# Kernel optimization log

Hardware: AMD Instinct MI355X
Metric: run time of the kernel (lower is better)

The kernel has to match this reference:

```python
import jax, jax.numpy as jnp
import numpy as np

NUM_HEADS = 16
ROPE_BASE = 10000.0


def _rope_cos_sin(T, head_dim, dtype):
    # standard rotary: angles[t, i] = t * base^(-2i/head_dim), half-split layout
    inv_freq = 1.0 / (ROPE_BASE ** (jnp.arange(0, head_dim, 2, dtype=jnp.float32) / head_dim))
    ang = jnp.arange(T, dtype=jnp.float32)[:, None] * inv_freq[None, :]  # [T, hd/2]
    cos = jnp.concatenate([jnp.cos(ang), jnp.cos(ang)], axis=-1).astype(dtype)  # [T, hd]
    sin = jnp.concatenate([jnp.sin(ang), jnp.sin(ang)], axis=-1).astype(dtype)
    return cos, sin


def _rotate_half(t):
    t1, t2 = jnp.split(t, 2, axis=-1)
    return jnp.concatenate([-t2, t1], axis=-1)


def _apply_rope(t, cos, sin):
    # t: [B, H, T, hd]; cos/sin: [T, hd]
    return t * cos[None, None] + _rotate_half(t) * sin[None, None]


def setup_inputs() -> dict:
    key = jax.random.key(0)
    B, T, C = 2, 2048, 1024
    k1, k2, k3 = jax.random.split(key, 3)
    x = jax.random.normal(k1, (B, T, C), dtype=jnp.float32)
    w_attn = jax.random.normal(k2, (C, 3 * C), dtype=jnp.float32) * (C ** -0.5)
    w_proj = jax.random.normal(k3, (C, C), dtype=jnp.float32) * (C ** -0.5)
    return {"x": x, "w_attn": w_attn, "w_proj": w_proj}


def reference(x, w_attn, w_proj):
    B, T, C = x.shape
    H = NUM_HEADS
    hd = C // H

    qkv = x @ w_attn  # [B, T, 3C]
    q, k, v = jnp.split(qkv, 3, axis=-1)
    # [B, T, C] -> [B, H, T, hd]
    q = q.reshape(B, T, H, hd).transpose(0, 2, 1, 3)
    k = k.reshape(B, T, H, hd).transpose(0, 2, 1, 3)
    v = v.reshape(B, T, H, hd).transpose(0, 2, 1, 3)

    cos, sin = _rope_cos_sin(T, hd, x.dtype)
    q = _apply_rope(q, cos, sin)
    k = _apply_rope(k, cos, sin)

    scale = 1.0 / np.sqrt(hd).astype(np.float32)
    att = jnp.einsum('bhqd,bhkd->bhqk', q, k) * scale  # [B, H, T, T]
    causal = jnp.tril(jnp.ones((T, T), dtype=bool))
    att = jnp.where(causal[None, None], att, jnp.array(-jnp.inf, dtype=att.dtype))
    att = jax.nn.softmax(att, axis=-1)
    y = jnp.einsum('bhqk,bhkd->bhqd', att, v)  # [B, H, T, hd]
    y = y.transpose(0, 2, 1, 3).reshape(B, T, C)
    return y @ w_proj
```

## Files before the change

### kernel.cpp

```cpp
#include <hip/hip_runtime.h>

typedef unsigned short u16;
typedef unsigned int u32;
typedef unsigned long long u64;
typedef __attribute__((ext_vector_type(8))) short s16x8;
typedef __attribute__((ext_vector_type(8))) __bf16 bf16x8;
typedef __attribute__((ext_vector_type(4))) float fx4;
typedef __attribute__((ext_vector_type(16))) float fx16;
typedef __attribute__((ext_vector_type(2))) u32 u32x2;
typedef __attribute__((ext_vector_type(4))) u32 u32x4;

__device__ __forceinline__ fx4 mfma_16x16x32(s16x8 a, s16x8 b, fx4 c) {
  return __builtin_amdgcn_mfma_f32_16x16x32_bf16(
      __builtin_bit_cast(bf16x8, a), __builtin_bit_cast(bf16x8, b), c, 0, 0, 0);
}
__device__ __forceinline__ fx16 mfma_32x32x16(s16x8 a, s16x8 b, fx16 c) {
  return __builtin_amdgcn_mfma_f32_32x32x16_bf16(
      __builtin_bit_cast(bf16x8, a), __builtin_bit_cast(bf16x8, b), c, 0, 0, 0);
}

__device__ __forceinline__ u16 f2bf(float f) {
  u32 u = __builtin_bit_cast(u32, f);
  u32 r = u + 0x7fffu + ((u >> 16) & 1u);
  return (u16)(r >> 16);
}
__device__ __forceinline__ float bf2f(u16 h) {
  u32 u = ((u32)h) << 16;
  return __builtin_bit_cast(float, u);
}

__device__ __forceinline__ u32 cvtpk(float lo, float hi) {
  u32 r;
  asm("v_cvt_pk_bf16_f32 %0, %1, %2" : "=v"(r) : "v"(lo), "v"(hi));
  return r;
}

__device__ __forceinline__ float max3f(float a, float b, float c) {
  float r;
  asm("v_max3_f32 %0, %1, %2, %3" : "=v"(r) : "v"(a), "v"(b), "v"(c));
  return r;
}

__device__ __forceinline__ void plswap(u32& x, u32& y) {
  typedef __attribute__((ext_vector_type(2))) unsigned int uix2;
  uix2 r = __builtin_amdgcn_permlane32_swap(x, y, false, false);
  x = r[0];
  y = r[1];
}

__device__ __forceinline__ float xhalf_max(float v) {
  u32 a = __builtin_bit_cast(u32, v), b = a;
  plswap(a, b);
  return fmaxf(__builtin_bit_cast(float, a), __builtin_bit_cast(float, b));
}
__device__ __forceinline__ float xhalf_sum(float v) {
  u32 a = __builtin_bit_cast(u32, v), b = a;
  plswap(a, b);
  return __builtin_bit_cast(float, a) + __builtin_bit_cast(float, b);
}

__device__ __forceinline__ void gload16(const void* g, void* l) {
  __builtin_amdgcn_global_load_lds(
      (const __attribute__((address_space(1))) u32*)g,
      (__attribute__((address_space(3))) u32*)l, 16, 0, 0);
}

#define B_ 2
#define T_ 2048
#define C_ 1024
#define H_ 16
#define HD_ 64
#define BH_ 32
#define M_ 4096
#define CF_ 0.18033688011112042f

__global__ void rope_table_k(float* __restrict__ ct, float* __restrict__ st) {
  int id = blockIdx.x * 256 + threadIdx.x;
  int t = id >> 5, i = id & 31;
  float f = exp2f(-(float)i * (13.287712379549449f / 32.0f));
  float a = (float)t * f;
  float s, c;
  sincosf(a, &s, &c);
  ct[id] = c;
  st[id] = s;
}

__global__ void cvt_f32_bf16_k(const float* __restrict__ in, u16* __restrict__ outp) {
  int id = blockIdx.x * 256 + threadIdx.x;
  const fx4* p = (const fx4*)(in + (u64)id * 8);
  fx4 v0 = p[0], v1 = p[1];
  s16x8 r;
#pragma unroll
  for (int j = 0; j < 4; ++j) {
    r[j] = (short)f2bf(v0[j]);
    r[4 + j] = (short)f2bf(v1[j]);
  }
  *((s16x8*)outp + id) = r;
}

__global__ void transpose_w_k(const float* __restrict__ W, u16* __restrict__ WT,
                              int Ncols, int R) {
  __shared__ u16 T_s[64 * 72];
  int c0 = blockIdx.x * 64, r0 = blockIdx.y * 64;
  int tid = threadIdx.x;
#pragma unroll
  for (int it = 0; it < 4; ++it) {
    int idx = it * 256 + tid;
    int r = idx >> 4, c4 = (idx & 15) * 4;
    fx4 v = *(const fx4*)(W + (u64)(r0 + r) * Ncols + c0 + c4);
#pragma unroll
    for (int j = 0; j < 4; ++j) T_s[(c4 + j) * 72 + r] = f2bf(v[j]);
  }
  __syncthreads();
#pragma unroll
  for (int it = 0; it < 2; ++it) {
    int idx = it * 256 + tid;
    int rc = idx >> 3, c8 = (idx & 7) * 8;
    s16x8 v = *(const s16x8*)(T_s + rc * 72 + c8);
    *(s16x8*)(WT + (u64)(c0 + rc) * R + r0 + c8) = v;
  }
}

template <int EPI>
__global__ __launch_bounds__(256, 2) void gemm_bt_k(
    const u16* __restrict__ A, const u16* __restrict__ B, float* __restrict__ C,
    u16* __restrict__ Qo, u16* __restrict__ Ko, u16* __restrict__ Vo,
    const float* __restrict__ ct, const float* __restrict__ st,
    int M, int N, int K) {
  __shared__ u16 As[128 * 32];
  __shared__ u16 Bs[128 * 32];
  int tid = threadIdx.x, lane = tid & 63, w = tid >> 6;
  int wm = w >> 1, wn = w & 1, l15 = lane & 15, l4 = lane >> 4;
  int nwg = gridDim.x * gridDim.y;
  int id = blockIdx.y * gridDim.x + blockIdx.x;
  int qq = nwg >> 3;
  id = (id & 7) * qq + (id >> 3);
  int m0 = (id / gridDim.x) * 128, n0 = (id % gridDim.x) * 128;
  fx4 acc[4][4] = {};
  int arow = tid >> 2, ac8 = (tid & 3) * 8;
  const u16* Ab = A + (u64)(m0 + arow) * K + ac8;
  const u16* Bb = B + (u64)(n0 + arow) * K + ac8;
  char* AsB = (char*)As + tid * 16;
  char* BsB = (char*)Bs + tid * 16;

  for (int k0 = 0; k0 < K; k0 += 32) {
    __syncthreads();
    gload16(Ab + k0, AsB);
    gload16(Ab + (u64)64 * K + k0, AsB + 4096);
    gload16(Bb + k0, BsB);
    gload16(Bb + (u64)64 * K + k0, BsB + 4096);
    __syncthreads();
    s16x8 a[4], b[4];
#pragma unroll
    for (int mi = 0; mi < 4; ++mi)
      a[mi] = *(const s16x8*)((const char*)As + (wm * 64 + mi * 16 + l15) * 64 + l4 * 16);
#pragma unroll
    for (int ni = 0; ni < 4; ++ni)
      b[ni] = *(const s16x8*)((const char*)Bs + (wn * 64 + ni * 16 + l15) * 64 + l4 * 16);
#pragma unroll
    for (int mi = 0; mi < 4; ++mi)
#pragma unroll
      for (int ni = 0; ni < 4; ++ni)
        acc[mi][ni] = mfma_16x16x32(a[mi], b[ni], acc[mi][ni]);
  }

  if (EPI == 0) {
#pragma unroll
    for (int mi = 0; mi < 4; ++mi)
#pragma unroll
      for (int ni = 0; ni < 4; ++ni)
#pragma unroll
        for (int r = 0; r < 4; ++r) {
          u64 row = (u64)(m0 + wm * 64 + mi * 16 + l4 * 4 + r);
          int col = n0 + wn * 64 + ni * 16 + l15;
          C[row * N + col] = acc[mi][ni][r];
        }
  } else {
#pragma unroll
    for (int mi = 0; mi < 4; ++mi)
#pragma unroll
      for (int r = 0; r < 4; ++r) {
        int row = m0 + wm * 64 + mi * 16 + l4 * 4 + r;
        int b2 = row >> 11, t = row & (T_ - 1);
#pragma unroll
        for (int ni = 0; ni < 2; ++ni) {
          int col = n0 + wn * 64 + ni * 16 + l15;
          int qi = col >> 10, h = (col >> 6) & 15, d = ni * 16 + l15;
          float lo = acc[mi][ni][r], hi = acc[mi][ni + 2][r];
          if (qi == 2) {
            u64 vbase =
                ((((u64)(b2 * H_ + h)) * (T_ / 8) + (t >> 3)) * HD_ + d) * 8 + (t & 7);
            Vo[vbase] = f2bf(lo);
            Vo[vbase + 32 * 8] = f2bf(hi);
          } else {
            float c = ct[t * 32 + d], s = st[t * 32 + d];
            float sc = (qi == 0) ? CF_ : 1.0f;
            u16* dst = (qi == 0) ? Qo : Ko;
            u64 base = ((((u64)(b2 * H_ + h)) * 8 + (d >> 3)) * T_ + t) * 8 + (d & 7);
            dst[base] = f2bf((lo * c - hi * s) * sc);
            dst[base + (u64)4 * T_ * 8] = f2bf((hi * c + lo * s) * sc);
          }
        }
      }
  }
}


#define LOADK(KC, KVI)                                                 \
  do {                                                                 \
    _Pragma("unroll")                                                  \
    for (int ks_ = 0; ks_ < 4; ++ks_)                                  \
      KC[ks_] = *(const s16x8*)(kp[ks_] + (u64)(KVI) * 256);           \
  } while (0)

#define LOADV(VC, KVI)                                                 \
  do {                                                                 \
    const u16* vk_ = vpb + (u64)(KVI) * 2048;                          \
    VC[0] = *(const s16x8*)(vk_);                                      \
    VC[1] = *(const s16x8*)(vk_ + 256);                                \
    VC[2] = *(const s16x8*)(vk_ + 1024);                               \
    VC[3] = *(const s16x8*)(vk_ + 1280);                               \
  } while (0)

#define ATTN_STEP(KC, VC, KVI)                                                \
  do {                                                                        \
    fx16 s_ = {};                                                             \
    __builtin_amdgcn_s_setprio(1);                                            \
    _Pragma("unroll")                                                         \
    for (int ks_ = 0; ks_ < 4; ++ks_)                                         \
      s_ = mfma_32x32x16(KC[ks_], qf[ks_], s_);                               \
    __builtin_amdgcn_s_setprio(0);                                            \
    if ((KVI) == jt) {                                                        \
      _Pragma("unroll")                                                       \
      for (int r_ = 0; r_ < 16; ++r_) {                                       \
        int cr_ = (r_ & 3) + 8 * (r_ >> 2) + 4 * h;                           \
        s_[r_] = (cr_ > ql) ? -1e30f : s_[r_];                                \
      }                                                                       \
    }                                                                         \
    float u0_ = max3f(s_[0], s_[1], s_[2]);                                   \
    float u1_ = max3f(s_[3], s_[4], s_[5]);                                   \
    float u2_ = max3f(s_[6], s_[7], s_[8]);                                   \
    float u3_ = max3f(s_[9], s_[10], s_[11]);                                 \
    float u4_ = max3f(s_[12], s_[13], s_[14]);                                \
    float v0_ = max3f(u0_, u1_, s_[15]);                                      \
    float v1_ = max3f(u2_, u3_, u4_);                                         \
    float rowmax_ = xhalf_max(fmaxf(v0_, v1_));                               \
    if (!__all(rowmax_ <= m + 8.f)) {                                         \
      float mnew_ = fmaxf(m, rowmax_);                                        \
      float corr_ = exp2f(m - mnew_);                                         \
      l *= corr_;                                                             \
      oL *= corr_;                                                            \
      oH *= corr_;                                                            \
      m = mnew_;                                                              \
    }                                                                         \
    float p_[16];                                                             \
    _Pragma("unroll")                                                         \
    for (int r_ = 0; r_ < 16; ++r_) p_[r_] = exp2f(s_[r_] - m);               \
    float a0_ = (p_[0] + p_[8]) + (p_[1] + p_[9]);                            \
    float a1_ = (p_[2] + p_[10]) + (p_[3] + p_[11]);                          \
    float a2_ = (p_[4] + p_[12]) + (p_[5] + p_[13]);                          \
    float a3_ = (p_[6] + p_[14]) + (p_[7] + p_[15]);                          \
    l += xhalf_sum((a0_ + a1_) + (a2_ + a3_));                                \
    u32 x0_ = cvtpk(p_[0], p_[1]), x1_ = cvtpk(p_[2], p_[3]);                 \
    u32 y0_ = cvtpk(p_[4], p_[5]), y1_ = cvtpk(p_[6], p_[7]);                 \
    plswap(x0_, y0_);                                                         \
    plswap(x1_, y1_);                                                         \
    u32x4 f0w_ = {x0_, x1_, y0_, y1_};                                        \
    u32 x2_ = cvtpk(p_[8], p_[9]), x3_ = cvtpk(p_[10], p_[11]);               \
    u32 y2_ = cvtpk(p_[12], p_[13]), y3_ = cvtpk(p_[14], p_[15]);             \
    plswap(x2_, y2_);                                                         \
    plswap(x3_, y3_);                                                         \
    u32x4 f1w_ = {x2_, x3_, y2_, y3_};                                        \
    s16x8 pf0_ = __builtin_bit_cast(s16x8, f0w_);                             \
    s16x8 pf1_ = __builtin_bit_cast(s16x8, f1w_);                             \
    __builtin_amdgcn_s_setprio(1);                                            \
    oL = mfma_32x32x16(VC[0], pf0_, oL);                                      \
    oH = mfma_32x32x16(VC[1], pf0_, oH);                                      \
    oL = mfma_32x32x16(VC[2], pf1_, oL);                                      \
    oH = mfma_32x32x16(VC[3], pf1_, oH);                                      \
    __builtin_amdgcn_s_setprio(0);                                            \
  } while (0)

#define OSTRIDE 68

__global__ __launch_bounds__(256, 3) void attn_fwd_k(
    const u16* __restrict__ Qp, const u16* __restrict__ Kp,
    const u16* __restrict__ Vp, u16* __restrict__ Y) {
  __shared__ float Ob[4 * 32 * OSTRIDE];
  __shared__ float Ml[4 * 32 * 2];
  int tid = threadIdx.x, lane = tid & 63, w = tid >> 6;
  int ql = lane & 31, h = lane >> 5;
  int bh = blockIdx.x & 31;
  int jt = 63 - (blockIdx.x >> 5);
  int q0 = jt * 32;
  int b2 = bh >> 4, head = bh & 15;
  int n = jt + 1;
  int lo = (w * n) >> 2, hi = ((w + 1) * n) >> 2;

  s16x8 qf[4];
#pragma unroll
  for (int ks = 0; ks < 4; ++ks)
    qf[ks] = *(const s16x8*)(Qp + (((u64)bh * 8 + ks * 2 + h) * T_ + q0 + ql) * 8);

  const u16* kp[4];
#pragma unroll
  for (int ks = 0; ks < 4; ++ks)
    kp[ks] = Kp + (((u64)bh * 8 + ks * 2 + h) * T_ + ql) * 8;
  const u16* vpb = Vp + (((u64)bh * (T_ / 8) + h) * HD_ + ql) * 8;

  fx16 oL = {}, oH = {};
  float m = -1e30f, l = 0.f;

  if (lo < hi) {
    s16x8 kA[4], vA[4], kB[4], vB[4];
    LOADK(kA, lo);
    LOADV(vA, lo);
    int kv = lo;
    for (; kv + 1 < hi; kv += 2) {
      LOADK(kB, kv + 1);
      LOADV(vB, kv + 1);
      ATTN_STEP(kA, vA, kv);
      if (kv + 2 < hi) {
        LOADK(kA, kv + 2);
        LOADV(vA, kv + 2);
      }
      ATTN_STEP(kB, vB, kv + 1);
    }
    if (kv < hi) ATTN_STEP(kA, vA, kv);
  }

  {
    float* ob = Ob + (w * 32 + ql) * OSTRIDE;
#pragma unroll
    for (int g = 0; g < 4; ++g) {
      fx4 a = {oL[4 * g], oL[4 * g + 1], oL[4 * g + 2], oL[4 * g + 3]};
      *(fx4*)(ob + 8 * g + 4 * h) = a;
      fx4 b = {oH[4 * g], oH[4 * g + 1], oH[4 * g + 2], oH[4 * g + 3]};
      *(fx4*)(ob + 32 + 8 * g + 4 * h) = b;
    }
    if (h == 0) {
      Ml[(w * 32 + ql) * 2] = m;
      Ml[(w * 32 + ql) * 2 + 1] = l;
    }
  }
  __syncthreads();

  {
    int q = tid >> 3, db = tid & 7;
    float mm0 = Ml[(0 * 32 + q) * 2], ll0 = Ml[(0 * 32 + q) * 2 + 1];
    float mm1 = Ml[(1 * 32 + q) * 2], ll1 = Ml[(1 * 32 + q) * 2 + 1];
    float mm2 = Ml[(2 * 32 + q) * 2], ll2 = Ml[(2 * 32 + q) * 2 + 1];
    float mm3 = Ml[(3 * 32 + q) * 2], ll3 = Ml[(3 * 32 + q) * 2 + 1];
    float mo = fmaxf(fmaxf(mm0, mm1), fmaxf(mm2, mm3));
    float w0 = exp2f(mm0 - mo), w1 = exp2f(mm1 - mo);
    float w2 = exp2f(mm2 - mo), w3 = exp2f(mm3 - mo);
    float rl = 1.0f / (ll0 * w0 + ll1 * w1 + ll2 * w2 + ll3 * w3);
    w0 *= rl; w1 *= rl; w2 *= rl; w3 *= rl;
    const float* ob = Ob + q * OSTRIDE + db * 8;
    fx4 aa = {}, bb = {};
#pragma unroll
    for (int i = 0; i < 4; ++i) {
      float wi = (i == 0) ? w0 : (i == 1) ? w1 : (i == 2) ? w2 : w3;
      fx4 pa = *(const fx4*)(ob + i * 32 * OSTRIDE);
      fx4 pb = *(const fx4*)(ob + i * 32 * OSTRIDE + 4);
      aa += wi * pa;
      bb += wi * pb;
    }
    u32x4 ow;
    ow[0] = cvtpk(aa[0], aa[1]);
    ow[1] = cvtpk(aa[2], aa[3]);
    ow[2] = cvtpk(bb[0], bb[1]);
    ow[3] = cvtpk(bb[2], bb[3]);
    int t = q0 + q;
    *(u32x4*)(Y + ((u64)(b2 * T_ + t)) * C_ + head * HD_ + db * 8) = ow;
  }
}

extern "C" void kernel_launch(void* const* d_in, const int* in_sizes, int n_in,
                              void* d_out, int out_size, void* d_ws, size_t ws_size,
                              hipStream_t stream) {
  (void)in_sizes; (void)n_in; (void)out_size; (void)ws_size;
  const float* x = (const float*)d_in[0];
  const float* w_attn = (const float*)d_in[1];
  const float* w_proj = (const float*)d_in[2];
  float* out = (float*)d_out;

  u16* xb = (u16*)d_ws;
  u16* waT = xb + (u64)M_ * C_;
  u16* wpT = waT + (u64)3 * C_ * C_;
  u16* Qp = wpT + (u64)C_ * C_;
  u16* Kp = Qp + (u64)BH_ * T_ * HD_;
  u16* Vp = Kp + (u64)BH_ * T_ * HD_;
  float* ct = (float*)(Vp + (u64)BH_ * T_ * HD_);
  float* st = ct + T_ * 32;
  u16* yb = xb;

  rope_table_k<<<256, 256, 0, stream>>>(ct, st);
  cvt_f32_bf16_k<<<(M_ * C_ / 8) / 256, 256, 0, stream>>>(x, xb);
  transpose_w_k<<<dim3(48, 16), 256, 0, stream>>>(w_attn, waT, 3 * C_, C_);
  transpose_w_k<<<dim3(16, 16), 256, 0, stream>>>(w_proj, wpT, C_, C_);

  gemm_bt_k<1><<<dim3(24, 32), 256, 0, stream>>>(xb, waT, nullptr, Qp, Kp, Vp,
                                                 ct, st, M_, 3 * C_, C_);

  attn_fwd_k<<<2048, 256, 0, stream>>>(Qp, Kp, Vp, yb);

  gemm_bt_k<0><<<dim3(8, 32), 256, 0, stream>>>(yb, wpT, out, nullptr, nullptr,
                                                nullptr, nullptr, nullptr,
                                                M_, C_, C_);
}
```

Measured before the change: 121.0 us.

## Double-buffer GEMM LDS tiles with BK=64 and XOR-swizzled layout

Restructures the bf16 GEMM main loop to use two LDS buffers with a 64-wide K tile. The next tile is prefetched while MFMAs run on the current one, so there is one barrier per iteration instead of two. The shared-memory layout is XOR-swizzled to avoid bank conflicts on the fragment reads. LDS use grows to 64 KB per block, which may limit the two-blocks-per-CU occupancy target.

```diff
diff --git a/kernel.cpp b/kernel.cpp
--- a/kernel.cpp
+++ b/kernel.cpp
@@ -127,8 +127,8 @@
     u16* __restrict__ Qo, u16* __restrict__ Ko, u16* __restrict__ Vo,
     const float* __restrict__ ct, const float* __restrict__ st,
     int M, int N, int K) {
-  __shared__ u16 As[128 * 32];
-  __shared__ u16 Bs[128 * 32];
+  __shared__ u16 As[2][128 * 64];
+  __shared__ u16 Bs[2][128 * 64];
   int tid = threadIdx.x, lane = tid & 63, w = tid >> 6;
   int wm = w >> 1, wn = w & 1, l15 = lane & 15, l4 = lane >> 4;
   int nwg = gridDim.x * gridDim.y;
@@ -137,32 +137,58 @@
   id = (id & 7) * qq + (id >> 3);
   int m0 = (id / gridDim.x) * 128, n0 = (id % gridDim.x) * 128;
   fx4 acc[4][4] = {};
-  int arow = tid >> 2, ac8 = (tid & 3) * 8;
-  const u16* Ab = A + (u64)(m0 + arow) * K + ac8;
-  const u16* Bb = B + (u64)(n0 + arow) * K + ac8;
-  char* AsB = (char*)As + tid * 16;
-  char* BsB = (char*)Bs + tid * 16;
-
-  for (int k0 = 0; k0 < K; k0 += 32) {
+
+  int srow = tid >> 3;
+  int sslot = (tid & 7) ^ (srow & 7);
+  const u16* Ab = A + (u64)(m0 + srow) * K + sslot * 8;
+  const u16* Bb = B + (u64)(n0 + srow) * K + sslot * 8;
+
+#define GSTAGE(BUF, KOFF)                                                     \
+  do {                                                                        \
+    _Pragma("unroll")                                                         \
+    for (int g_ = 0; g_ < 4; ++g_) {                                          \
+      gload16(Ab + (KOFF) + (u64)(g_ * 32) * K,                               \
+              (char*)As[BUF] + g_ * 4096 + tid * 16);                         \
+      gload16(Bb + (KOFF) + (u64)(g_ * 32) * K,                               \
+              (char*)Bs[BUF] + g_ * 4096 + tid * 16);                         \
+    }                                                                         \
+  } while (0)
+
+#define GCOMP(BUF)                                                            \
+  do {                                                                        \
+    _Pragma("unroll")                                                         \
+    for (int kk_ = 0; kk_ < 2; ++kk_) {                                       \
+      s16x8 a_[4], b_[4];                                                     \
+      int sw_ = ((kk_ * 4 + l4) ^ (l15 & 7)) * 16;                            \
+      _Pragma("unroll")                                                       \
+      for (int mi_ = 0; mi_ < 4; ++mi_)                                       \
+        a_[mi_] = *(const s16x8*)((const char*)As[BUF] +                      \
+                                  (wm * 64 + mi_ * 16 + l15) * 128 + sw_);    \
+      _Pragma("unroll")                                                       \
+      for (int ni_ = 0; ni_ < 4; ++ni_)                                       \
+        b_[ni_] = *(const s16x8*)((const char*)Bs[BUF] +                      \
+                                  (wn * 64 + ni_ * 16 + l15) * 128 + sw_);    \
+      _Pragma("unroll")                                                       \
+      for (int mi_ = 0; mi_ < 4; ++mi_)                                       \
+        _Pragma("unroll")                                                     \
+        for (int ni_ = 0; ni_ < 4; ++ni_)                                     \
+          acc[mi_][ni_] = mfma_16x16x32(a_[mi_], b_[ni_], acc[mi_][ni_]);     \
+    }                                                                         \
+  } while (0)
+
+  int NT = K >> 6;
+  GSTAGE(0, 0);
+  __syncthreads();
+  int cur = 0;
+  for (int t = 0; t < NT - 1; ++t) {
+    GSTAGE(cur ^ 1, (t + 1) << 6);
+    GCOMP(cur);
     __syncthreads();
-    gload16(Ab + k0, AsB);
-    gload16(Ab + (u64)64 * K + k0, AsB + 4096);
-    gload16(Bb + k0, BsB);
-    gload16(Bb + (u64)64 * K + k0, BsB + 4096);
-    __syncthreads();
-    s16x8 a[4], b[4];
-#pragma unroll
-    for (int mi = 0; mi < 4; ++mi)
-      a[mi] = *(const s16x8*)((const char*)As + (wm * 64 + mi * 16 + l15) * 64 + l4 * 16);
-#pragma unroll
-    for (int ni = 0; ni < 4; ++ni)
-      b[ni] = *(const s16x8*)((const char*)Bs + (wn * 64 + ni * 16 + l15) * 64 + l4 * 16);
-#pragma unroll
-    for (int mi = 0; mi < 4; ++mi)
-#pragma unroll
-      for (int ni = 0; ni < 4; ++ni)
-        acc[mi][ni] = mfma_16x16x32(a[mi], b[ni], acc[mi][ni]);
-  }
+    cur ^= 1;
+  }
+  GCOMP(cur);
+#undef GSTAGE
+#undef GCOMP
 
   if (EPI == 0) {
 #pragma unroll
```

Measured after the change: 127.4 us. 5.3% more time.
